# Optimization experiments

Measured on AMD Instinct MI355X. Metric: run time of the kernel, lower is better.

The kernel has to match this reference:

```python
import jax, jax.numpy as jnp
import numpy as np


def setup_inputs() -> dict:
    key = jax.random.key(0)
    k1, k2 = jax.random.split(key)
    h = jax.random.normal(k1, (8, 16, 64, 512), dtype=jnp.float32)
    M = jax.random.normal(k2, (20000, 512), dtype=jnp.float32)
    return {"h": h, "M": M}


def reference(h, M):
    # h: [B, T, X, R], M: [K, R]
    B, T, X, R = h.shape
    hf = h.reshape(-1, R)                      # [N, R]
    att = jax.nn.softmax(hf @ M.T, axis=1)     # [N, K], unscaled dot-product
    out = att @ M                              # [N, R]
    return out.reshape(B, T, X, R)
```

## Files before the change

### kernel.cpp

```cpp
#include <hip/hip_runtime.h>
#include <stdint.h>

#define NQ 8192
#define NK 20000
#define RD 512
#define NT 157
#define TS0 79

typedef float f32x4 __attribute__((ext_vector_type(4)));
typedef short s16x8 __attribute__((ext_vector_type(8)));

__device__ __forceinline__ unsigned short bf16_rn(float x) {
    uint32_t u = __float_as_uint(x);
    return (unsigned short)((u + 0x7FFFu + ((u >> 16) & 1)) >> 16);
}

__device__ __forceinline__ void lds_barrier() {
    asm volatile("s_waitcnt lgkmcnt(0)\n\ts_barrier" ::: "memory");
}

__global__ void preconv_kernel(const float* __restrict__ M,
                               unsigned short* __restrict__ Mhi,
                               unsigned short* __restrict__ Mlo,
                               unsigned short* __restrict__ MT) {
    __shared__ float tilef[64 * 65];
    const int k0 = blockIdx.x * 64, r0 = blockIdx.y * 64;
    const int t = threadIdx.x;
#pragma unroll
    for (int i = 0; i < 16; i++) {
        int e = t + i * 256;
        int kr = e >> 6, cc = e & 63;
        int key = k0 + kr;
        if (key < NK) {
            float x = M[(size_t)key * RD + r0 + cc];
            uint32_t u = __float_as_uint(x);
            Mhi[(size_t)key * RD + r0 + cc] = (unsigned short)(u >> 16);
            Mlo[(size_t)key * RD + r0 + cc] = bf16_rn(x - __uint_as_float(u & 0xFFFF0000u));
            tilef[cc * 65 + kr] = x;
        }
    }
    __syncthreads();
#pragma unroll
    for (int i = 0; i < 16; i++) {
        int e = t + i * 256;
        int rr = e >> 6, kk = e & 63;
        int key = k0 + kk;
        if (key < NK) MT[(size_t)(r0 + rr) * NK + key] = bf16_rn(tilef[rr * 65 + kk]);
    }
}

__global__ __launch_bounds__(256, 2) void flash6_kernel(
        const float* __restrict__ h,
        const unsigned short* __restrict__ Mhi,
        const unsigned short* __restrict__ Mlo,
        const unsigned short* __restrict__ MT,
        float* __restrict__ out,
        float* __restrict__ Opart,
        float* __restrict__ mpart,
        float* __restrict__ lpart,
        int nsplit) {
    __shared__ unsigned short qbuf[32768];
    __shared__ unsigned short pbuf[8 * 512];
    __shared__ float smaxb[4 * 2 * 16];
    __shared__ float ssumb[4 * 2 * 16];

    const int tid = threadIdx.x;
    const int ch = tid >> 6, l = tid & 63;
    const int l15 = l & 15, q4 = l >> 4;
    const int kq = (l15 >> 3) & 1, jj = l15 & 7;

    int qb, split;
    if (nsplit == 2) { split = blockIdx.x & 1; qb = blockIdx.x >> 1; }
    else             { split = 0;              qb = blockIdx.x; }
    const int koff = (split == 0) ? 0 : TS0 * 128;
    const int ntl  = (nsplit == 2) ? ((split == 0) ? TS0 : (NT - TS0)) : NT;
    const int total_ks = ntl * 16;
    const int qbase = qb * 32;

    const size_t base_w = (size_t)(ch * 32 + l15) * RD + q4 * 8;
    auto kaddr = [&](int g, int cb) -> size_t {
        if (g >= total_ks) g = total_ks - 1;
        int t2 = g >> 4, s2 = g & 15;
        return (size_t)(koff + t2 * 128) * RD + (size_t)s2 * 32 + base_w + (size_t)cb * (16 * RD);
    };

    s16x8 kh[2][4], kl[2][4];
#pragma unroll
    for (int i = 0; i < 4; i++) {
        size_t a0 = kaddr(i, 0), a1 = kaddr(i, 1);
        kh[0][i] = *(const s16x8*)(Mhi + a0);
        kl[0][i] = *(const s16x8*)(Mlo + a0);
        kh[1][i] = *(const s16x8*)(Mhi + a1);
        kl[1][i] = *(const s16x8*)(Mlo + a1);
    }

#pragma unroll
    for (int i = 0; i < 8; i++) {
        int g = tid + i * 256;
        int row = g >> 6, s = (g >> 2) & 15, qg = g & 3;
        int strip = row >> 4, lrow = row & 15;
        const float* src = h + (size_t)(qbase + row) * RD + s * 32 + qg * 8;
        f32x4 a = *(const f32x4*)src;
        f32x4 b = *(const f32x4*)(src + 4);
        s16x8 hi8, lo8;
#pragma unroll
        for (int j = 0; j < 8; j++) {
            float x = (j < 4) ? a[j] : b[j - 4];
            uint32_t u = __float_as_uint(x);
            hi8[j] = (short)(u >> 16);
            lo8[j] = (short)bf16_rn(x - __uint_as_float(u & 0xFFFF0000u));
        }
        int off = ((strip * 16 + s) * 512 + (qg * 16 + lrow) * 8);
        *(s16x8*)&qbuf[off] = hi8;
        *(s16x8*)&qbuf[16384 + off] = lo8;
    }
    lds_barrier();

    f32x4 O[2][8];
#pragma unroll
    for (int st = 0; st < 2; st++)
#pragma unroll
        for (int ct = 0; ct < 8; ct++) O[st][ct] = 0.f;
    f32x4 m_run[2], l_run[2];
    m_run[0] = -3e38f; m_run[1] = -3e38f; l_run[0] = 0.f; l_run[1] = 0.f;

    for (int tile = 0; tile < ntl; tile++) {
        f32x4 C[2][2];
        C[0][0] = 0.f; C[0][1] = 0.f; C[1][0] = 0.f; C[1][1] = 0.f;
#pragma unroll
        for (int s = 0; s < 16; s++) {
            const int sl = s & 3;
            s16x8 kh0 = kh[0][sl], kl0 = kl[0][sl];
            s16x8 kh1 = kh[1][sl], kl1 = kl[1][sl];
            {
                int g = tile * 16 + s + 4;
                size_t a0 = kaddr(g, 0), a1 = kaddr(g, 1);
                kh[0][sl] = *(const s16x8*)(Mhi + a0);
                kl[0][sl] = *(const s16x8*)(Mlo + a0);
                kh[1][sl] = *(const s16x8*)(Mhi + a1);
                kl[1][sl] = *(const s16x8*)(Mlo + a1);
            }
#pragma unroll
            for (int st = 0; st < 2; st++) {
                s16x8 qh = *(const s16x8*)&qbuf[(st * 16 + s) * 512 + l * 8];
                s16x8 ql = *(const s16x8*)&qbuf[16384 + (st * 16 + s) * 512 + l * 8];
                C[st][0] = __builtin_amdgcn_mfma_f32_16x16x32_bf16(qh, kh0, C[st][0], 0, 0, 0);
                C[st][1] = __builtin_amdgcn_mfma_f32_16x16x32_bf16(qh, kh1, C[st][1], 0, 0, 0);
                C[st][0] = __builtin_amdgcn_mfma_f32_16x16x32_bf16(ql, kh0, C[st][0], 0, 0, 0);
                C[st][1] = __builtin_amdgcn_mfma_f32_16x16x32_bf16(ql, kh1, C[st][1], 0, 0, 0);
                C[st][0] = __builtin_amdgcn_mfma_f32_16x16x32_bf16(qh, kl0, C[st][0], 0, 0, 0);
                C[st][1] = __builtin_amdgcn_mfma_f32_16x16x32_bf16(qh, kl1, C[st][1], 0, 0, 0);
            }
        }
        if (tile == ntl - 1) {
#pragma unroll
            for (int cb = 0; cb < 2; cb++) {
                int kg = koff + tile * 128 + ch * 32 + cb * 16 + l15;
                if (kg >= NK) { C[0][cb] = -3e38f; C[1][cb] = -3e38f; }
            }
        }

        const unsigned short* mtp = MT + (size_t)(ch * 128 + l15) * NK + koff + tile * 128 + q4 * 8;
        s16x8 bt[2][4];
#pragma unroll
        for (int sk = 0; sk < 4; sk++) {
            bt[0][sk] = *(const s16x8*)(mtp + sk * 32);
            bt[1][sk] = *(const s16x8*)(mtp + (size_t)16 * NK + sk * 32);
        }

        f32x4 mx[2];
#pragma unroll
        for (int st = 0; st < 2; st++)
#pragma unroll
            for (int v = 0; v < 4; v++) mx[st][v] = fmaxf(C[st][0][v], C[st][1][v]);
#pragma unroll
        for (int d = 1; d < 16; d <<= 1) {
#pragma unroll
            for (int st = 0; st < 2; st++)
#pragma unroll
                for (int v = 0; v < 4; v++) mx[st][v] = fmaxf(mx[st][v], __shfl_xor(mx[st][v], d, 16));
        }
        if (l15 == 0) {
            *(f32x4*)&smaxb[(ch * 2 + 0) * 16 + q4 * 4] = mx[0];
            *(f32x4*)&smaxb[(ch * 2 + 1) * 16 + q4 * 4] = mx[1];
        }
        lds_barrier();
        f32x4 mnew[2]; mnew[0] = m_run[0]; mnew[1] = m_run[1];
#pragma unroll
        for (int cc = 0; cc < 4; cc++) {
#pragma unroll
            for (int st = 0; st < 2; st++) {
                f32x4 tv = *(const f32x4*)&smaxb[(cc * 2 + st) * 16 + q4 * 4];
#pragma unroll
                for (int v = 0; v < 4; v++) mnew[st][v] = fmaxf(mnew[st][v], tv[v]);
            }
        }
        f32x4 alpha[2];
#pragma unroll
        for (int st = 0; st < 2; st++)
#pragma unroll
            for (int v = 0; v < 4; v++) {
                alpha[st][v] = __expf(m_run[st][v] - mnew[st][v]);
                m_run[st][v] = mnew[st][v];
            }
        f32x4 ps[2]; ps[0] = 0.f; ps[1] = 0.f;
#pragma unroll
        for (int st = 0; st < 2; st++) {
#pragma unroll
            for (int cb = 0; cb < 2; cb++) {
#pragma unroll
                for (int v = 0; v < 4; v++) {
                    float p = __expf(C[st][cb][v] - mnew[st][v]);
                    ps[st][v] += p;
                    pbuf[(ch * 2 + st) * 512 + ((cb * 2 + kq) * 16 + q4 * 4 + v) * 8 + jj] = bf16_rn(p);
                }
            }
        }
#pragma unroll
        for (int d = 1; d < 16; d <<= 1) {
#pragma unroll
            for (int st = 0; st < 2; st++)
#pragma unroll
                for (int v = 0; v < 4; v++) ps[st][v] += __shfl_xor(ps[st][v], d, 16);
        }
        if (l15 == 0) {
            *(f32x4*)&ssumb[(ch * 2 + 0) * 16 + q4 * 4] = ps[0];
            *(f32x4*)&ssumb[(ch * 2 + 1) * 16 + q4 * 4] = ps[1];
        }
        lds_barrier();
        f32x4 ts[2]; ts[0] = 0.f; ts[1] = 0.f;
#pragma unroll
        for (int cc = 0; cc < 4; cc++) {
            ts[0] += *(const f32x4*)&ssumb[(cc * 2 + 0) * 16 + q4 * 4];
            ts[1] += *(const f32x4*)&ssumb[(cc * 2 + 1) * 16 + q4 * 4];
        }
#pragma unroll
        for (int st = 0; st < 2; st++)
#pragma unroll
            for (int v = 0; v < 4; v++) l_run[st][v] = l_run[st][v] * alpha[st][v] + ts[st][v];
#pragma unroll
        for (int st = 0; st < 2; st++)
#pragma unroll
            for (int ct = 0; ct < 8; ct++)
#pragma unroll
                for (int v = 0; v < 4; v++) O[st][ct][v] *= alpha[st][v];
        s16x8 pa[2][4];
#pragma unroll
        for (int st = 0; st < 2; st++)
#pragma unroll
            for (int sk = 0; sk < 4; sk++)
                pa[st][sk] = *(const s16x8*)&pbuf[((sk * 2 + st) * 512) + l * 8];

#pragma unroll
        for (int ct = 0; ct < 8; ct++) {
            s16x8 b0 = bt[ct & 1][0], b1 = bt[ct & 1][1], b2 = bt[ct & 1][2], b3 = bt[ct & 1][3];
            if (ct < 6) {
#pragma unroll
                for (int sk = 0; sk < 4; sk++)
                    bt[ct & 1][sk] = *(const s16x8*)(mtp + (size_t)(ct + 2) * 16 * NK + sk * 32);
            }
            O[0][ct] = __builtin_amdgcn_mfma_f32_16x16x32_bf16(pa[0][0], b0, O[0][ct], 0, 0, 0);
            O[1][ct] = __builtin_amdgcn_mfma_f32_16x16x32_bf16(pa[1][0], b0, O[1][ct], 0, 0, 0);
            O[0][ct] = __builtin_amdgcn_mfma_f32_16x16x32_bf16(pa[0][1], b1, O[0][ct], 0, 0, 0);
            O[1][ct] = __builtin_amdgcn_mfma_f32_16x16x32_bf16(pa[1][1], b1, O[1][ct], 0, 0, 0);
            O[0][ct] = __builtin_amdgcn_mfma_f32_16x16x32_bf16(pa[0][2], b2, O[0][ct], 0, 0, 0);
            O[1][ct] = __builtin_amdgcn_mfma_f32_16x16x32_bf16(pa[1][2], b2, O[1][ct], 0, 0, 0);
            O[0][ct] = __builtin_amdgcn_mfma_f32_16x16x32_bf16(pa[0][3], b3, O[0][ct], 0, 0, 0);
            O[1][ct] = __builtin_amdgcn_mfma_f32_16x16x32_bf16(pa[1][3], b3, O[1][ct], 0, 0, 0);
        }
        lds_barrier();
    }

    if (nsplit == 2) {
        float* Od = Opart + (size_t)split * NQ * RD;
#pragma unroll
        for (int st = 0; st < 2; st++)
#pragma unroll
            for (int ct = 0; ct < 8; ct++)
#pragma unroll
                for (int v = 0; v < 4; v++)
                    Od[(size_t)(qbase + st * 16 + q4 * 4 + v) * RD + ch * 128 + ct * 16 + l15] =
                        O[st][ct][v];
        if (ch == 0 && l15 == 0) {
#pragma unroll
            for (int st = 0; st < 2; st++)
#pragma unroll
                for (int v = 0; v < 4; v++) {
                    mpart[split * NQ + qbase + st * 16 + q4 * 4 + v] = m_run[st][v];
                    lpart[split * NQ + qbase + st * 16 + q4 * 4 + v] = l_run[st][v];
                }
        }
    } else {
#pragma unroll
        for (int st = 0; st < 2; st++)
#pragma unroll
            for (int ct = 0; ct < 8; ct++)
#pragma unroll
                for (int v = 0; v < 4; v++)
                    out[(size_t)(qbase + st * 16 + q4 * 4 + v) * RD + ch * 128 + ct * 16 + l15] =
                        O[st][ct][v] / l_run[st][v];
    }
}

__global__ __launch_bounds__(256) void combine_kernel(const float* __restrict__ Opart,
                                                      const float* __restrict__ mpart,
                                                      const float* __restrict__ lpart,
                                                      float* __restrict__ out) {
    const int t = threadIdx.x;
    const int row = blockIdx.x * 2 + (t >> 7);
    const int d = (t & 127) * 4;
    float m0 = mpart[row], m1 = mpart[NQ + row];
    float l0 = lpart[row], l1 = lpart[NQ + row];
    float m = fmaxf(m0, m1);
    float w0 = __expf(m0 - m), w1 = __expf(m1 - m);
    float inv = 1.f / (w0 * l0 + w1 * l1);
    f32x4 o0 = *(const f32x4*)&Opart[(size_t)row * RD + d];
    f32x4 o1 = *(const f32x4*)&Opart[(size_t)NQ * RD + (size_t)row * RD + d];
    f32x4 r;
#pragma unroll
    for (int v = 0; v < 4; v++) r[v] = (o0[v] * w0 + o1[v] * w1) * inv;
    *(f32x4*)&out[(size_t)row * RD + d] = r;
}

__global__ __launch_bounds__(256) void naive_kernel(const float* __restrict__ h,
                                                    const float* __restrict__ M,
                                                    float* __restrict__ out) {
    __shared__ float hs[16 * 520];
    __shared__ float ms[8 * 520];
    __shared__ float sdot[2][128];
    __shared__ float sm[16], sl[16], sal[16], sp[16][8];
    const int t = threadIdx.x;
    const int qbase = blockIdx.x * 16;
#pragma unroll
    for (int i = 0; i < 32; i++) {
        int e = t + i * 256;
        int row = e >> 9, col = e & 511;
        hs[row * 520 + col] = h[(size_t)(qbase + row) * RD + col];
    }
    if (t < 16) { sm[t] = -3e38f; sl[t] = 0.f; }
    float Oacc[32];
#pragma unroll
    for (int i = 0; i < 32; i++) Oacc[i] = 0.f;
    const int q = t >> 4;
    const int eb = (t & 15) * 32;

    for (int k0 = 0; k0 < NK; k0 += 8) {
        __syncthreads();
#pragma unroll
        for (int i = 0; i < 16; i++) {
            int e = t + i * 256;
            if (e < 4096) {
                int kk = e >> 9, col = e & 511;
                ms[kk * 520 + col] = M[(size_t)(k0 + kk) * RD + col];
            }
        }
        __syncthreads();
        {
            int pair = t & 127, half = t >> 7;
            int qq = pair & 15, kk = pair >> 4;
            const float* hp = &hs[qq * 520 + half * 256];
            const float* mp = &ms[kk * 520 + half * 256];
            float acc = 0.f;
#pragma unroll 8
            for (int e = 0; e < 256; e++) acc += hp[e] * mp[e];
            sdot[half][pair] = acc;
        }
        __syncthreads();
        if (t < 16) {
            int qq = t;
            float s8[8];
#pragma unroll
            for (int kk = 0; kk < 8; kk++) s8[kk] = sdot[0][qq + 16 * kk] + sdot[1][qq + 16 * kk];
            float mn = sm[qq];
#pragma unroll
            for (int kk = 0; kk < 8; kk++) mn = fmaxf(mn, s8[kk]);
            float al = __expf(sm[qq] - mn);
            float addl = 0.f;
#pragma unroll
            for (int kk = 0; kk < 8; kk++) { float p = __expf(s8[kk] - mn); sp[qq][kk] = p; addl += p; }
            sm[qq] = mn; sl[qq] = sl[qq] * al + addl; sal[qq] = al;
        }
        __syncthreads();
        {
            float al = sal[q];
#pragma unroll
            for (int i = 0; i < 32; i++) Oacc[i] *= al;
#pragma unroll
            for (int kk = 0; kk < 8; kk++) {
                float p = sp[q][kk];
                const float* mp = &ms[kk * 520 + eb];
#pragma unroll
                for (int i = 0; i < 32; i++) Oacc[i] += p * mp[i];
            }
        }
    }
    __syncthreads();
    float inv = 1.f / sl[q];
#pragma unroll
    for (int i = 0; i < 32; i++) out[(size_t)(qbase + q) * RD + eb + i] = Oacc[i] * inv;
}

extern "C" void kernel_launch(void* const* d_in, const int* in_sizes, int n_in,
                              void* d_out, int out_size, void* d_ws, size_t ws_size,
                              hipStream_t stream) {
    const float* h = (const float*)d_in[0];
    const float* M = (const float*)d_in[1];
    float* out = (float*)d_out;
    const size_t seg = (size_t)NK * RD;
    const size_t base_bytes = (seg * 3ull + 8192ull) * 2ull;
    const size_t opart_bytes = 2ull * NQ * RD * 4ull;
    const size_t stat_bytes = 2ull * 2ull * NQ * 4ull;
    const size_t need_split = base_bytes + opart_bytes + stat_bytes;

    if (ws_size >= base_bytes) {
        unsigned short* Mhi = (unsigned short*)d_ws;
        unsigned short* Mlo = Mhi + seg;
        unsigned short* MT  = Mlo + seg;
        float* Opart = (float*)((char*)d_ws + base_bytes);
        float* mpart = Opart + 2ull * NQ * RD;
        float* lpart = mpart + 2ull * NQ;
        preconv_kernel<<<dim3(313, 8), 256, 0, stream>>>(M, Mhi, Mlo, MT);
        if (ws_size >= need_split) {
            flash6_kernel<<<512, 256, 0, stream>>>(h, Mhi, Mlo, MT, out, Opart, mpart, lpart, 2);
            combine_kernel<<<NQ / 2, 256, 0, stream>>>(Opart, mpart, lpart, out);
        } else {
            flash6_kernel<<<256, 256, 0, stream>>>(h, Mhi, Mlo, MT, out, Opart, mpart, lpart, 1);
        }
    } else {
        naive_kernel<<<512, 256, 0, stream>>>(h, M, out);
    }
}
```

Measured before the change: 1.593 ms.

## Restructure PV loop order, shrink K prefetch depth, drop trailing tile barrier

Measured after the change: 1.536 ms. -3.5%, faster.

```diff
diff --git a/kernel.cpp b/kernel.cpp
--- a/kernel.cpp
+++ b/kernel.cpp
@@ -49,7 +49,32 @@
     }
 }
 
-__global__ __launch_bounds__(256, 2) void flash6_kernel(
+#define S_STEP(ii, s_) do {                                                                        \
+        const int sl_ = (s_) & 1;                                                                  \
+        s16x8 kh0_ = kh[0][sl_], kl0_ = kl[0][sl_];                                                \
+        s16x8 kh1_ = kh[1][sl_], kl1_ = kl[1][sl_];                                                \
+        {                                                                                          \
+            int g_ = (ii) * 16 + (s_) + 2;                                                         \
+            size_t a0_ = kaddr(g_, 0), a1_ = kaddr(g_, 1);                                         \
+            kh[0][sl_] = *(const s16x8*)(Mhi + a0_);                                               \
+            kl[0][sl_] = *(const s16x8*)(Mlo + a0_);                                               \
+            kh[1][sl_] = *(const s16x8*)(Mhi + a1_);                                               \
+            kl[1][sl_] = *(const s16x8*)(Mlo + a1_);                                               \
+        }                                                                                          \
+        _Pragma("unroll")                                                                          \
+        for (int st_ = 0; st_ < 2; st_++) {                                                       \
+            s16x8 qh_ = *(const s16x8*)&qbuf[(st_ * 16 + (s_)) * 512 + l * 8];                     \
+            s16x8 ql_ = *(const s16x8*)&qbuf[16384 + (st_ * 16 + (s_)) * 512 + l * 8];             \
+            C[st_][0] = __builtin_amdgcn_mfma_f32_16x16x32_bf16(qh_, kh0_, C[st_][0], 0, 0, 0);    \
+            C[st_][1] = __builtin_amdgcn_mfma_f32_16x16x32_bf16(qh_, kh1_, C[st_][1], 0, 0, 0);    \
+            C[st_][0] = __builtin_amdgcn_mfma_f32_16x16x32_bf16(ql_, kh0_, C[st_][0], 0, 0, 0);    \
+            C[st_][1] = __builtin_amdgcn_mfma_f32_16x16x32_bf16(ql_, kh1_, C[st_][1], 0, 0, 0);    \
+            C[st_][0] = __builtin_amdgcn_mfma_f32_16x16x32_bf16(qh_, kl0_, C[st_][0], 0, 0, 0);    \
+            C[st_][1] = __builtin_amdgcn_mfma_f32_16x16x32_bf16(qh_, kl1_, C[st_][1], 0, 0, 0);    \
+        }                                                                                          \
+    } while (0)
+
+__global__ __launch_bounds__(256, 2) void flash12_kernel(
         const float* __restrict__ h,
         const unsigned short* __restrict__ Mhi,
         const unsigned short* __restrict__ Mlo,
@@ -84,9 +109,9 @@
         return (size_t)(koff + t2 * 128) * RD + (size_t)s2 * 32 + base_w + (size_t)cb * (16 * RD);
     };
 
-    s16x8 kh[2][4], kl[2][4];
-#pragma unroll
-    for (int i = 0; i < 4; i++) {
+    s16x8 kh[2][2], kl[2][2];
+#pragma unroll
+    for (int i = 0; i < 2; i++) {
         size_t a0 = kaddr(i, 0), a1 = kaddr(i, 1);
         kh[0][i] = *(const s16x8*)(Mhi + a0);
         kl[0][i] = *(const s16x8*)(Mlo + a0);
@@ -128,30 +153,7 @@
         f32x4 C[2][2];
         C[0][0] = 0.f; C[0][1] = 0.f; C[1][0] = 0.f; C[1][1] = 0.f;
 #pragma unroll
-        for (int s = 0; s < 16; s++) {
-            const int sl = s & 3;
-            s16x8 kh0 = kh[0][sl], kl0 = kl[0][sl];
-            s16x8 kh1 = kh[1][sl], kl1 = kl[1][sl];
-            {
-                int g = tile * 16 + s + 4;
-                size_t a0 = kaddr(g, 0), a1 = kaddr(g, 1);
-                kh[0][sl] = *(const s16x8*)(Mhi + a0);
-                kl[0][sl] = *(const s16x8*)(Mlo + a0);
-                kh[1][sl] = *(const s16x8*)(Mhi + a1);
-                kl[1][sl] = *(const s16x8*)(Mlo + a1);
-            }
-#pragma unroll
-            for (int st = 0; st < 2; st++) {
-                s16x8 qh = *(const s16x8*)&qbuf[(st * 16 + s) * 512 + l * 8];
-                s16x8 ql = *(const s16x8*)&qbuf[16384 + (st * 16 + s) * 512 + l * 8];
-                C[st][0] = __builtin_amdgcn_mfma_f32_16x16x32_bf16(qh, kh0, C[st][0], 0, 0, 0);
-                C[st][1] = __builtin_amdgcn_mfma_f32_16x16x32_bf16(qh, kh1, C[st][1], 0, 0, 0);
-                C[st][0] = __builtin_amdgcn_mfma_f32_16x16x32_bf16(ql, kh0, C[st][0], 0, 0, 0);
-                C[st][1] = __builtin_amdgcn_mfma_f32_16x16x32_bf16(ql, kh1, C[st][1], 0, 0, 0);
-                C[st][0] = __builtin_amdgcn_mfma_f32_16x16x32_bf16(qh, kl0, C[st][0], 0, 0, 0);
-                C[st][1] = __builtin_amdgcn_mfma_f32_16x16x32_bf16(qh, kl1, C[st][1], 0, 0, 0);
-            }
-        }
+        for (int s = 0; s < 16; s++) S_STEP(tile, s);
         if (tile == ntl - 1) {
 #pragma unroll
             for (int cb = 0; cb < 2; cb++) {
@@ -161,11 +163,11 @@
         }
 
         const unsigned short* mtp = MT + (size_t)(ch * 128 + l15) * NK + koff + tile * 128 + q4 * 8;
-        s16x8 bt[2][4];
-#pragma unroll
-        for (int sk = 0; sk < 4; sk++) {
-            bt[0][sk] = *(const s16x8*)(mtp + sk * 32);
-            bt[1][sk] = *(const s16x8*)(mtp + (size_t)16 * NK + sk * 32);
+        s16x8 btg[2][8];
+#pragma unroll
+        for (int ct = 0; ct < 8; ct++) {
+            btg[0][ct] = *(const s16x8*)(mtp + (size_t)ct * 16 * NK);
+            btg[1][ct] = *(const s16x8*)(mtp + (size_t)ct * 16 * NK + 32);
         }
 
         f32x4 mx[2];
@@ -244,31 +246,35 @@
             for (int ct = 0; ct < 8; ct++)
 #pragma unroll
                 for (int v = 0; v < 4; v++) O[st][ct][v] *= alpha[st][v];
-        s16x8 pa[2][4];
-#pragma unroll
-        for (int st = 0; st < 2; st++)
-#pragma unroll
-            for (int sk = 0; sk < 4; sk++)
-                pa[st][sk] = *(const s16x8*)&pbuf[((sk * 2 + st) * 512) + l * 8];
-
-#pragma unroll
-        for (int ct = 0; ct < 8; ct++) {
-            s16x8 b0 = bt[ct & 1][0], b1 = bt[ct & 1][1], b2 = bt[ct & 1][2], b3 = bt[ct & 1][3];
-            if (ct < 6) {
-#pragma unroll
-                for (int sk = 0; sk < 4; sk++)
-                    bt[ct & 1][sk] = *(const s16x8*)(mtp + (size_t)(ct + 2) * 16 * NK + sk * 32);
-            }
-            O[0][ct] = __builtin_amdgcn_mfma_f32_16x16x32_bf16(pa[0][0], b0, O[0][ct], 0, 0, 0);
-            O[1][ct] = __builtin_amdgcn_mfma_f32_16x16x32_bf16(pa[1][0], b0, O[1][ct], 0, 0, 0);
-            O[0][ct] = __builtin_amdgcn_mfma_f32_16x16x32_bf16(pa[0][1], b1, O[0][ct], 0, 0, 0);
-            O[1][ct] = __builtin_amdgcn_mfma_f32_16x16x32_bf16(pa[1][1], b1, O[1][ct], 0, 0, 0);
-            O[0][ct] = __builtin_amdgcn_mfma_f32_16x16x32_bf16(pa[0][2], b2, O[0][ct], 0, 0, 0);
-            O[1][ct] = __builtin_amdgcn_mfma_f32_16x16x32_bf16(pa[1][2], b2, O[1][ct], 0, 0, 0);
-            O[0][ct] = __builtin_amdgcn_mfma_f32_16x16x32_bf16(pa[0][3], b3, O[0][ct], 0, 0, 0);
-            O[1][ct] = __builtin_amdgcn_mfma_f32_16x16x32_bf16(pa[1][3], b3, O[1][ct], 0, 0, 0);
-        }
-        lds_barrier();
+
+#pragma unroll
+        for (int sk = 0; sk < 4; sk++) {
+            s16x8 pa0 = *(const s16x8*)&pbuf[((sk * 2 + 0) * 512) + l * 8];
+            s16x8 pa1 = *(const s16x8*)&pbuf[((sk * 2 + 1) * 512) + l * 8];
+            s16x8 b0 = btg[sk & 1][0], b1 = btg[sk & 1][1], b2 = btg[sk & 1][2], b3 = btg[sk & 1][3];
+            s16x8 b4 = btg[sk & 1][4], b5 = btg[sk & 1][5], b6 = btg[sk & 1][6], b7 = btg[sk & 1][7];
+            if (sk < 2) {
+#pragma unroll
+                for (int ct = 0; ct < 8; ct++)
+                    btg[sk & 1][ct] = *(const s16x8*)(mtp + (size_t)ct * 16 * NK + (sk + 2) * 32);
+            }
+            O[0][0] = __builtin_amdgcn_mfma_f32_16x16x32_bf16(pa0, b0, O[0][0], 0, 0, 0);
+            O[1][0] = __builtin_amdgcn_mfma_f32_16x16x32_bf16(pa1, b0, O[1][0], 0, 0, 0);
+            O[0][1] = __builtin_amdgcn_mfma_f32_16x16x32_bf16(pa0, b1, O[0][1], 0, 0, 0);
+            O[1][1] = __builtin_amdgcn_mfma_f32_16x16x32_bf16(pa1, b1, O[1][1], 0, 0, 0);
+            O[0][2] = __builtin_amdgcn_mfma_f32_16x16x32_bf16(pa0, b2, O[0][2], 0, 0, 0);
+            O[1][2] = __builtin_amdgcn_mfma_f32_16x16x32_bf16(pa1, b2, O[1][2], 0, 0, 0);
+            O[0][3] = __builtin_amdgcn_mfma_f32_16x16x32_bf16(pa0, b3, O[0][3], 0, 0, 0);
+            O[1][3] = __builtin_amdgcn_mfma_f32_16x16x32_bf16(pa1, b3, O[1][3], 0, 0, 0);
+            O[0][4] = __builtin_amdgcn_mfma_f32_16x16x32_bf16(pa0, b4, O[0][4], 0, 0, 0);
+            O[1][4] = __builtin_amdgcn_mfma_f32_16x16x32_bf16(pa1, b4, O[1][4], 0, 0, 0);
+            O[0][5] = __builtin_amdgcn_mfma_f32_16x16x32_bf16(pa0, b5, O[0][5], 0, 0, 0);
+            O[1][5] = __builtin_amdgcn_mfma_f32_16x16x32_bf16(pa1, b5, O[1][5], 0, 0, 0);
+            O[0][6] = __builtin_amdgcn_mfma_f32_16x16x32_bf16(pa0, b6, O[0][6], 0, 0, 0);
+            O[1][6] = __builtin_amdgcn_mfma_f32_16x16x32_bf16(pa1, b6, O[1][6], 0, 0, 0);
+            O[0][7] = __builtin_amdgcn_mfma_f32_16x16x32_bf16(pa0, b7, O[0][7], 0, 0, 0);
+            O[1][7] = __builtin_amdgcn_mfma_f32_16x16x32_bf16(pa1, b7, O[1][7], 0, 0, 0);
+        }
     }
 
     if (nsplit == 2) {
@@ -421,10 +427,10 @@
         float* lpart = mpart + 2ull * NQ;
         preconv_kernel<<<dim3(313, 8), 256, 0, stream>>>(M, Mhi, Mlo, MT);
         if (ws_size >= need_split) {
-            flash6_kernel<<<512, 256, 0, stream>>>(h, Mhi, Mlo, MT, out, Opart, mpart, lpart, 2);
+            flash12_kernel<<<512, 256, 0, stream>>>(h, Mhi, Mlo, MT, out, Opart, mpart, lpart, 2);
             combine_kernel<<<NQ / 2, 256, 0, stream>>>(Opart, mpart, lpart, out);
         } else {
-            flash6_kernel<<<256, 256, 0, stream>>>(h, Mhi, Mlo, MT, out, Opart, mpart, lpart, 1);
+            flash12_kernel<<<256, 256, 0, stream>>>(h, Mhi, Mlo, MT, out, Opart, mpart, lpart, 1);
         }
     } else {
         naive_kernel<<<512, 256, 0, stream>>>(h, M, out);
```
